# Kernel tuning notes

Measured on AMD Instinct MI355X. Metric: run time of the kernel, lower is better.

The kernel has to match this reference:

```python
import jax, jax.numpy as jnp
import numpy as np

F = 64  # dim_features
DIM_TASK = 32


def setup_inputs() -> dict:
    key = jax.random.key(0)
    ks = jax.random.split(key, 16)
    n_state, n_task, n_actor = 65536, 32768, 32768
    E_st, E_ta = 2_000_000, 1_000_000
    inp = {
        'x_state': jax.random.normal(ks[0], (n_state, F), jnp.float32),
        'x_task': jax.random.normal(ks[1], (n_task, F), jnp.float32),
        'x_actor': jax.random.normal(ks[2], (n_actor, F), jnp.float32),
        'edge_attr': jax.random.normal(ks[3], (E_st, 2), jnp.float32),
        # GINEConv edge linear: Linear(2 -> F)
        'We': jax.random.normal(ks[4], (2, F), jnp.float32) * 0.5,
        'be': jnp.zeros((F,), jnp.float32),
        # GinStandardMLP: Linear(F,F) -> ReLU -> Linear(F,F)
        'W1a': jax.random.normal(ks[5], (F, F), jnp.float32) / np.sqrt(F),
        'b1a': jnp.zeros((F,), jnp.float32),
        'W1b': jax.random.normal(ks[6], (F, F), jnp.float32) / np.sqrt(F),
        'b1b': jnp.zeros((F,), jnp.float32),
        # UnactivatedMLP: Linear(F,F) -> ReLU -> Linear(F,1)
        'W2a': jax.random.normal(ks[7], (F, F), jnp.float32) / np.sqrt(F),
        'b2a': jnp.zeros((F,), jnp.float32),
        'W2b': jax.random.normal(ks[8], (F, 1), jnp.float32) / np.sqrt(F),
        'b2b': jnp.zeros((1,), jnp.float32),
        'src_st': jax.random.randint(ks[9], (E_st,), 0, n_state, jnp.int32),
        'dst_st': jax.random.randint(ks[10], (E_st,), 0, n_task, jnp.int32),
        'src_ta': jax.random.randint(ks[11], (E_ta,), 0, n_task, jnp.int32),
        'dst_ta': jax.random.randint(ks[12], (E_ta,), 0, n_actor, jnp.int32),
    }
    return inp


def reference(x_state, x_task, x_actor, edge_attr, We, be, W1a, b1a, W1b, b1b,
              W2a, b2a, W2b, b2b, src_st, dst_st, src_ta, dst_ta):
    n_task = x_task.shape[0]
    n_actor = x_actor.shape[0]
    # --- GINEConv (eps=0): agg_i = sum_e relu(x_src[e] + lin(edge_attr[e])) ---
    msg = jax.nn.relu(x_state[src_st] + edge_attr @ We + be)  # [E_st, F]
    agg = jax.ops.segment_sum(msg, dst_st, num_segments=n_task)  # [n_task, F]
    h = x_task + agg  # (1+eps)*x_r + agg, eps=0
    # GinStandardMLP: Linear-ReLU-Linear
    x1 = jax.nn.relu(h @ W1a + b1a) @ W1b + b1b  # [n_task, F]
    # --- GINConv (eps=0): agg2_i = sum_e x1[src[e]] ---
    agg2 = jax.ops.segment_sum(x1[src_ta], dst_ta, num_segments=n_actor)  # [n_actor, F]
    h2 = x_actor + agg2
    # UnactivatedMLP: Linear-ReLU-Linear -> 1
    logits = jax.nn.relu(h2 @ W2a + b2a) @ W2b + b2b  # [n_actor, 1]
    return logits.reshape(-1, DIM_TASK)
```

## Files before the change

kernel.cpp:

```cpp
#include <hip/hip_runtime.h>

#define F 64
#define TILE 4096
#define NB 1024
#define ROWSB 32
#define CAP1 2560
#define CAP2 1408

typedef __attribute__((ext_vector_type(8))) short bf8;
typedef __attribute__((ext_vector_type(4))) float f4;
typedef __attribute__((ext_vector_type(2))) float fl2;

__device__ __forceinline__ unsigned short f2bf(float f) {
    unsigned u = __float_as_uint(f);
    unsigned r = u + 0x7fffu + ((u >> 16) & 1u);
    return (unsigned short)(r >> 16);
}
__device__ __forceinline__ float bf2f(unsigned short h) {
    return __uint_as_float((unsigned)h << 16);
}
__device__ __forceinline__ fl2 unpack2(unsigned d) {
    fl2 r;
    r.x = __uint_as_float(d << 16);
    r.y = __uint_as_float(d & 0xffff0000u);
    return r;
}

__global__ __launch_bounds__(1024) void prep_kernel(
    const float4* __restrict__ xs4, ushort4* __restrict__ xsb4, int n4,
    const int* __restrict__ src1, const int* __restrict__ dst1,
    const float* __restrict__ ea, int E1,
    int* __restrict__ cur1, uint2* __restrict__ keyA1,
    const int* __restrict__ src2, const int* __restrict__ dst2, int E2,
    int* __restrict__ cur2, unsigned* __restrict__ keyA2,
    int nCvt, int nBin1)
{
    __shared__ uint2 stage[TILE];
    __shared__ int hist[NB], scanb[NB], lstart[NB], lcur[NB], gbase[NB];
    int bid = blockIdx.x;
    int tid = threadIdx.x;

    if (bid < nCvt) {
        int i = bid * 1024 + tid;
        if (i < n4) {
            float4 v = xs4[i];
            ushort4 o;
            o.x = f2bf(v.x); o.y = f2bf(v.y); o.z = f2bf(v.z); o.w = f2bf(v.w);
            xsb4[i] = o;
        }
        return;
    }

    if (bid < nCvt + nBin1) {
        int base = (bid - nCvt) * TILE;
        int cnt = min(TILE, E1 - base);
        hist[tid] = 0;
        __syncthreads();
        int myb[4];
        #pragma unroll
        for (int j = 0; j < 4; ++j) {
            int idx = tid + 1024 * j;
            if (idx < cnt) {
                int b = dst1[base + idx] >> 5;
                myb[j] = b;
                atomicAdd(&hist[b], 1);
            } else myb[j] = -1;
        }
        __syncthreads();
        int c = hist[tid];
        gbase[tid] = CAP1 * tid + atomicAdd(&cur1[tid], c);
        scanb[tid] = c;
        __syncthreads();
        for (int off = 1; off < NB; off <<= 1) {
            int u = (tid >= off) ? scanb[tid - off] : 0;
            __syncthreads();
            scanb[tid] += u;
            __syncthreads();
        }
        int excl = scanb[tid] - c;
        lstart[tid] = excl;
        lcur[tid] = excl;
        __syncthreads();
        #pragma unroll
        for (int j = 0; j < 4; ++j) {
            int idx = tid + 1024 * j;
            if (idx < cnt) {
                int b = myb[j];
                int p = atomicAdd(&lcur[b], 1);
                float2 e2 = ((const float2* __restrict__)ea)[base + idx];
                unsigned sd = ((unsigned)src1[base + idx] << 16) | (unsigned)dst1[base + idx];
                unsigned pk = ((unsigned)f2bf(e2.y) << 16) | (unsigned)f2bf(e2.x);
                stage[p] = make_uint2(sd, pk);
            }
        }
        __syncthreads();
        #pragma unroll
        for (int j = 0; j < 4; ++j) {
            int p = tid + 1024 * j;
            if (p < cnt) {
                uint2 f = stage[p];
                int b = (int)(f.x & 0xffffu) >> 5;
                keyA1[gbase[b] + (p - lstart[b])] = f;
            }
        }
        return;
    }

    {
        unsigned* ustage = (unsigned*)stage;
        int base = (bid - nCvt - nBin1) * TILE;
        int cnt = min(TILE, E2 - base);
        hist[tid] = 0;
        __syncthreads();
        int myb[4];
        #pragma unroll
        for (int j = 0; j < 4; ++j) {
            int idx = tid + 1024 * j;
            if (idx < cnt) {
                int b = dst2[base + idx] >> 5;
                myb[j] = b;
                atomicAdd(&hist[b], 1);
            } else myb[j] = -1;
        }
        __syncthreads();
        int c = hist[tid];
        gbase[tid] = CAP2 * tid + atomicAdd(&cur2[tid], c);
        scanb[tid] = c;
        __syncthreads();
        for (int off = 1; off < NB; off <<= 1) {
            int u = (tid >= off) ? scanb[tid - off] : 0;
            __syncthreads();
            scanb[tid] += u;
            __syncthreads();
        }
        int excl = scanb[tid] - c;
        lstart[tid] = excl;
        lcur[tid] = excl;
        __syncthreads();
        #pragma unroll
        for (int j = 0; j < 4; ++j) {
            int idx = tid + 1024 * j;
            if (idx < cnt) {
                int b = myb[j];
                int p = atomicAdd(&lcur[b], 1);
                ustage[p] = ((unsigned)src2[base + idx] << 16) | (unsigned)dst2[base + idx];
            }
        }
        __syncthreads();
        #pragma unroll
        for (int j = 0; j < 4; ++j) {
            int p = tid + 1024 * j;
            if (p < cnt) {
                unsigned f = ustage[p];
                int b = (int)(f & 0xffffu) >> 5;
                keyA2[gbase[b] + (p - lstart[b])] = f;
            }
        }
    }
}

__global__ __launch_bounds__(512) void sg1_kernel(
    const uint2* __restrict__ keyA,
    const ushort* __restrict__ xsb,
    const float* __restrict__ x_task,
    const float* __restrict__ We, const float* __restrict__ be,
    const int* __restrict__ gcursor,
    float* __restrict__ hout, int n)
{
    __shared__ uint2 lpay[CAP1];
    __shared__ int hh[ROWSB], rst[ROWSB], cur[ROWSB];
    __shared__ float hbuf[8][F + 4];
    int tid = threadIdx.x;
    int b = blockIdx.x;
    int cnt = min(gcursor[b], CAP1);
    const uint2* ka = keyA + (size_t)b * CAP1;

    if (tid < ROWSB) hh[tid] = 0;
    __syncthreads();

    uint2 myk[5];
    #pragma unroll
    for (int j = 0; j < 5; ++j) {
        int idx = tid + 512 * j;
        if (idx < cnt) {
            myk[j] = ka[idx];
            atomicAdd(&hh[myk[j].x & 31u], 1);
        }
    }
    __syncthreads();
    if (tid < ROWSB) cur[tid] = hh[tid];
    __syncthreads();
    for (int off = 1; off < ROWSB; off <<= 1) {
        int u = (tid < ROWSB && tid >= off) ? cur[tid - off] : 0;
        __syncthreads();
        if (tid < ROWSB) cur[tid] += u;
        __syncthreads();
    }
    if (tid < ROWSB) {
        int excl = cur[tid] - hh[tid];
        rst[tid] = excl;
        cur[tid] = excl;
    }
    __syncthreads();
    #pragma unroll
    for (int j = 0; j < 5; ++j) {
        int idx = tid + 512 * j;
        if (idx < cnt) {
            int p = atomicAdd(&cur[myk[j].x & 31u], 1);
            lpay[p] = myk[j];
        }
    }
    __syncthreads();

    int wave = tid >> 6, lane = tid & 63;
    int q = lane & 7, g = lane >> 3;
    fl2 w0p[4], w1p[4], bbp[4];
    {
        float4 a0 = ((const float4* __restrict__)We)[q * 2];
        float4 a1 = ((const float4* __restrict__)We)[q * 2 + 1];
        float4 c0 = ((const float4* __restrict__)(We + F))[q * 2];
        float4 c1 = ((const float4* __restrict__)(We + F))[q * 2 + 1];
        float4 d0 = ((const float4* __restrict__)be)[q * 2];
        float4 d1 = ((const float4* __restrict__)be)[q * 2 + 1];
        w0p[0] = (fl2){a0.x, a0.y}; w0p[1] = (fl2){a0.z, a0.w};
        w0p[2] = (fl2){a1.x, a1.y}; w0p[3] = (fl2){a1.z, a1.w};
        w1p[0] = (fl2){c0.x, c0.y}; w1p[1] = (fl2){c0.z, c0.w};
        w1p[2] = (fl2){c1.x, c1.y}; w1p[3] = (fl2){c1.z, c1.w};
        bbp[0] = (fl2){d0.x, d0.y}; bbp[1] = (fl2){d0.z, d0.w};
        bbp[2] = (fl2){d1.x, d1.y}; bbp[3] = (fl2){d1.z, d1.w};
    }
    const fl2 zero2 = {0.f, 0.f};

    for (int r = wave; r < ROWSB; r += 8) {
        int row = b * ROWSB + r;
        if (row >= n) break;
        int start = rst[r];
        int c = hh[r];
        fl2 acc2[4];
        #pragma unroll
        for (int p = 0; p < 4; ++p) acc2[p] = zero2;

        #define SG1_BODY(ii)                                                     \
        {                                                                        \
            uint2 pe = lpay[start + (ii)];                                       \
            int s = (int)(pe.x >> 16);                                           \
            fl2 ex = {__uint_as_float(pe.y << 16), __uint_as_float(pe.y << 16)}; \
            fl2 ey = {__uint_as_float(pe.y & 0xffff0000u),                       \
                      __uint_as_float(pe.y & 0xffff0000u)};                      \
            uint4 xw = ((const uint4* __restrict__)(xsb + (size_t)s * F))[q];    \
            fl2 cc, t;                                                           \
            cc = __builtin_elementwise_fma(ey, w1p[0], bbp[0]);                  \
            cc = __builtin_elementwise_fma(ex, w0p[0], cc);                      \
            t = unpack2(xw.x) + cc;                                              \
            acc2[0] += __builtin_elementwise_max(t, zero2);                      \
            cc = __builtin_elementwise_fma(ey, w1p[1], bbp[1]);                  \
            cc = __builtin_elementwise_fma(ex, w0p[1], cc);                      \
            t = unpack2(xw.y) + cc;                                              \
            acc2[1] += __builtin_elementwise_max(t, zero2);                      \
            cc = __builtin_elementwise_fma(ey, w1p[2], bbp[2]);                  \
            cc = __builtin_elementwise_fma(ex, w0p[2], cc);                      \
            t = unpack2(xw.z) + cc;                                              \
            acc2[2] += __builtin_elementwise_max(t, zero2);                      \
            cc = __builtin_elementwise_fma(ey, w1p[3], bbp[3]);                  \
            cc = __builtin_elementwise_fma(ex, w0p[3], cc);                      \
            t = unpack2(xw.w) + cc;                                              \
            acc2[3] += __builtin_elementwise_max(t, zero2);                      \
        }

        int i = g;
        for (; i + 8 < c; i += 16) { SG1_BODY(i); SG1_BODY(i + 8); }
        for (; i < c; i += 8) SG1_BODY(i);
        #undef SG1_BODY

        float acc[8];
        #pragma unroll
        for (int p = 0; p < 4; ++p) { acc[2 * p] = acc2[p].x; acc[2 * p + 1] = acc2[p].y; }
        #pragma unroll
        for (int j = 0; j < 8; ++j) {
            acc[j] += __shfl_xor(acc[j], 8);
            acc[j] += __shfl_xor(acc[j], 16);
            acc[j] += __shfl_xor(acc[j], 32);
        }
        if (g == 0) {
            #pragma unroll
            for (int j = 0; j < 8; ++j)
                hbuf[wave][q * 8 + j] = acc[j];
        }
        float h = hbuf[wave][lane] + x_task[(size_t)row * F + lane];
        hout[(size_t)row * F + lane] = h;
    }
}

__global__ __launch_bounds__(256) void mlp1_kernel(
    const float* __restrict__ hin,
    const float* __restrict__ W1a, const float* __restrict__ b1a,
    const float* __restrict__ W1b, const float* __restrict__ b1b,
    ushort* __restrict__ x1b, int n)
{
    __shared__ float ldsH[4][16 * 68];
    int tid = threadIdx.x;
    int wave = tid >> 6, lane = tid & 63;
    int quad = lane >> 4, col = lane & 15;
    int rowbase = blockIdx.x * 64 + wave * 16;
    if (rowbase >= n) return;
    float* ltile = ldsH[wave];

    bf8 Wah[2][4], Wal[2][4], Wbh[2][4], Wbl[2][4];
    float ba1[4], bb1[4];
    #pragma unroll
    for (int kh = 0; kh < 2; ++kh)
        #pragma unroll
        for (int c = 0; c < 4; ++c) {
            bf8 th, tl, sh, sl;
            #pragma unroll
            for (int j = 0; j < 8; ++j) {
                int k = kh * 32 + quad * 8 + j;
                float wa = W1a[k * F + c * 16 + col];
                unsigned short h1 = f2bf(wa);
                th[j] = (short)h1; tl[j] = (short)f2bf(wa - bf2f(h1));
                float wb = W1b[k * F + c * 16 + col];
                unsigned short h2 = f2bf(wb);
                sh[j] = (short)h2; sl[j] = (short)f2bf(wb - bf2f(h2));
            }
            Wah[kh][c] = th; Wal[kh][c] = tl;
            Wbh[kh][c] = sh; Wbl[kh][c] = sl;
        }
    #pragma unroll
    for (int c = 0; c < 4; ++c) { ba1[c] = b1a[c * 16 + col]; bb1[c] = b1b[c * 16 + col]; }

    const float* hrow = hin + (size_t)(rowbase + col) * F + quad * 8;
    bf8 Ah[2], Al[2];
    #pragma unroll
    for (int kh = 0; kh < 2; ++kh) {
        bf8 th, tl;
        #pragma unroll
        for (int j = 0; j < 8; ++j) {
            float a = hrow[kh * 32 + j];
            unsigned short h1 = f2bf(a);
            th[j] = (short)h1; tl[j] = (short)f2bf(a - bf2f(h1));
        }
        Ah[kh] = th; Al[kh] = tl;
    }

    #pragma unroll
    for (int c = 0; c < 4; ++c) {
        f4 acc = {0.f, 0.f, 0.f, 0.f};
        #pragma unroll
        for (int kh = 0; kh < 2; ++kh) {
            acc = __builtin_amdgcn_mfma_f32_16x16x32_bf16(Ah[kh], Wah[kh][c], acc, 0, 0, 0);
            acc = __builtin_amdgcn_mfma_f32_16x16x32_bf16(Ah[kh], Wal[kh][c], acc, 0, 0, 0);
            acc = __builtin_amdgcn_mfma_f32_16x16x32_bf16(Al[kh], Wah[kh][c], acc, 0, 0, 0);
        }
        #pragma unroll
        for (int r = 0; r < 4; ++r)
            ltile[(quad * 4 + r) * 68 + c * 16 + col] = fmaxf(acc[r] + ba1[c], 0.f);
    }
    bf8 A2h[2], A2l[2];
    #pragma unroll
    for (int kh = 0; kh < 2; ++kh) {
        bf8 th, tl;
        #pragma unroll
        for (int j = 0; j < 8; ++j) {
            float a = ltile[col * 68 + kh * 32 + quad * 8 + j];
            unsigned short h1 = f2bf(a);
            th[j] = (short)h1; tl[j] = (short)f2bf(a - bf2f(h1));
        }
        A2h[kh] = th; A2l[kh] = tl;
    }
    #pragma unroll
    for (int c = 0; c < 4; ++c) {
        f4 acc = {0.f, 0.f, 0.f, 0.f};
        #pragma unroll
        for (int kh = 0; kh < 2; ++kh) {
            acc = __builtin_amdgcn_mfma_f32_16x16x32_bf16(A2h[kh], Wbh[kh][c], acc, 0, 0, 0);
            acc = __builtin_amdgcn_mfma_f32_16x16x32_bf16(A2h[kh], Wbl[kh][c], acc, 0, 0, 0);
            acc = __builtin_amdgcn_mfma_f32_16x16x32_bf16(A2l[kh], Wbh[kh][c], acc, 0, 0, 0);
        }
        #pragma unroll
        for (int r = 0; r < 4; ++r)
            ltile[(quad * 4 + r) * 68 + c * 16 + col] = acc[r] + bb1[c];
    }
    int rr = lane >> 2, cc = (lane & 3) * 16;
    unsigned o[8];
    #pragma unroll
    for (int j = 0; j < 8; ++j) {
        unsigned lo = f2bf(ltile[rr * 68 + cc + 2 * j]);
        unsigned hi = f2bf(ltile[rr * 68 + cc + 2 * j + 1]);
        o[j] = lo | (hi << 16);
    }
    uint4* dst = (uint4*)(x1b + (size_t)(rowbase + rr) * F + cc);
    dst[0] = make_uint4(o[0], o[1], o[2], o[3]);
    dst[1] = make_uint4(o[4], o[5], o[6], o[7]);
}

__global__ __launch_bounds__(512) void sg2_kernel(
    const unsigned* __restrict__ keyA,
    const ushort* __restrict__ x1b,
    const float* __restrict__ x_actor,
    const int* __restrict__ gcursor,
    float* __restrict__ h2out, int n)
{
    __shared__ unsigned lpay[CAP2];
    __shared__ int hh[ROWSB], rst[ROWSB], cur[ROWSB];
    __shared__ float hbuf[8][F + 4];
    int tid = threadIdx.x;
    int b = blockIdx.x;
    int cnt = min(gcursor[b], CAP2);
    const unsigned* ka = keyA + (size_t)b * CAP2;

    if (tid < ROWSB) hh[tid] = 0;
    __syncthreads();

    unsigned myk[3];
    #pragma unroll
    for (int j = 0; j < 3; ++j) {
        int idx = tid + 512 * j;
        if (idx < cnt) {
            myk[j] = ka[idx];
            atomicAdd(&hh[myk[j] & 31u], 1);
        }
    }
    __syncthreads();
    if (tid < ROWSB) cur[tid] = hh[tid];
    __syncthreads();
    for (int off = 1; off < ROWSB; off <<= 1) {
        int u = (tid < ROWSB && tid >= off) ? cur[tid - off] : 0;
        __syncthreads();
        if (tid < ROWSB) cur[tid] += u;
        __syncthreads();
    }
    if (tid < ROWSB) {
        int excl = cur[tid] - hh[tid];
        rst[tid] = excl;
        cur[tid] = excl;
    }
    __syncthreads();
    #pragma unroll
    for (int j = 0; j < 3; ++j) {
        int idx = tid + 512 * j;
        if (idx < cnt) {
            int p = atomicAdd(&cur[myk[j] & 31u], 1);
            lpay[p] = myk[j];
        }
    }
    __syncthreads();

    int wave = tid >> 6, lane = tid & 63;
    int q = lane & 7, g = lane >> 3;
    const fl2 zero2 = {0.f, 0.f};
    for (int r = wave; r < ROWSB; r += 8) {
        int row = b * ROWSB + r;
        if (row >= n) break;
        int start = rst[r];
        int c = hh[r];
        fl2 acc2[4];
        #pragma unroll
        for (int p = 0; p < 4; ++p) acc2[p] = zero2;

        #define SG2_BODY(ii)                                                  \
        {                                                                     \
            unsigned sd = lpay[start + (ii)];                                 \
            int s = (int)(sd >> 16);                                          \
            uint4 xw = ((const uint4* __restrict__)(x1b + (size_t)s * F))[q]; \
            acc2[0] += unpack2(xw.x);                                         \
            acc2[1] += unpack2(xw.y);                                         \
            acc2[2] += unpack2(xw.z);                                         \
            acc2[3] += unpack2(xw.w);                                         \
        }

        int i = g;
        for (; i + 8 < c; i += 16) { SG2_BODY(i); SG2_BODY(i + 8); }
        for (; i < c; i += 8) SG2_BODY(i);
        #undef SG2_BODY

        float acc[8];
        #pragma unroll
        for (int p = 0; p < 4; ++p) { acc[2 * p] = acc2[p].x; acc[2 * p + 1] = acc2[p].y; }
        #pragma unroll
        for (int j = 0; j < 8; ++j) {
            acc[j] += __shfl_xor(acc[j], 8);
            acc[j] += __shfl_xor(acc[j], 16);
            acc[j] += __shfl_xor(acc[j], 32);
        }
        if (g == 0) {
            #pragma unroll
            for (int j = 0; j < 8; ++j)
                hbuf[wave][q * 8 + j] = acc[j];
        }
        float h = hbuf[wave][lane] + x_actor[(size_t)row * F + lane];
        h2out[(size_t)row * F + lane] = h;
    }
}

__global__ __launch_bounds__(256) void mlp2_kernel(
    const float* __restrict__ h2in,
    const float* __restrict__ W2a, const float* __restrict__ b2a,
    const float* __restrict__ W2b, const float* __restrict__ b2b,
    float* __restrict__ out, int n)
{
    int tid = threadIdx.x;
    int wave = tid >> 6, lane = tid & 63;
    int quad = lane >> 4, col = lane & 15;
    int rowbase = blockIdx.x * 64 + wave * 16;
    if (rowbase >= n) return;

    bf8 Wah[2][4], Wal[2][4];
    float ba1[4], wo[4];
    #pragma unroll
    for (int kh = 0; kh < 2; ++kh)
        #pragma unroll
        for (int c = 0; c < 4; ++c) {
            bf8 th, tl;
            #pragma unroll
            for (int j = 0; j < 8; ++j) {
                int k = kh * 32 + quad * 8 + j;
                float w = W2a[k * F + c * 16 + col];
                unsigned short h1 = f2bf(w);
                th[j] = (short)h1; tl[j] = (short)f2bf(w - bf2f(h1));
            }
            Wah[kh][c] = th; Wal[kh][c] = tl;
        }
    #pragma unroll
    for (int c = 0; c < 4; ++c) { ba1[c] = b2a[c * 16 + col]; wo[c] = W2b[c * 16 + col]; }
    float bias2 = b2b[0];

    const float* hrow = h2in + (size_t)(rowbase + col) * F + quad * 8;
    bf8 Ah[2], Al[2];
    #pragma unroll
    for (int kh = 0; kh < 2; ++kh) {
        bf8 th, tl;
        #pragma unroll
        for (int j = 0; j < 8; ++j) {
            float a = hrow[kh * 32 + j];
            unsigned short h1 = f2bf(a);
            th[j] = (short)h1; tl[j] = (short)f2bf(a - bf2f(h1));
        }
        Ah[kh] = th; Al[kh] = tl;
    }

    float partial[4] = {0.f, 0.f, 0.f, 0.f};
    #pragma unroll
    for (int c = 0; c < 4; ++c) {
        f4 acc = {0.f, 0.f, 0.f, 0.f};
        #pragma unroll
        for (int kh = 0; kh < 2; ++kh) {
            acc = __builtin_amdgcn_mfma_f32_16x16x32_bf16(Ah[kh], Wah[kh][c], acc, 0, 0, 0);
            acc = __builtin_amdgcn_mfma_f32_16x16x32_bf16(Ah[kh], Wal[kh][c], acc, 0, 0, 0);
            acc = __builtin_amdgcn_mfma_f32_16x16x32_bf16(Al[kh], Wah[kh][c], acc, 0, 0, 0);
        }
        #pragma unroll
        for (int r = 0; r < 4; ++r)
            partial[r] += fmaxf(acc[r] + ba1[c], 0.f) * wo[c];
    }
    #pragma unroll
    for (int off = 1; off < 16; off <<= 1)
        #pragma unroll
        for (int r = 0; r < 4; ++r)
            partial[r] += __shfl_xor(partial[r], off);
    if (col == 0) {
        #pragma unroll
        for (int r = 0; r < 4; ++r)
            out[rowbase + quad * 4 + r] = partial[r] + bias2;
    }
}

extern "C" void kernel_launch(void* const* d_in, const int* in_sizes, int n_in,
                              void* d_out, int out_size, void* d_ws, size_t ws_size,
                              hipStream_t stream)
{
    const float* x_state   = (const float*)d_in[0];
    const float* x_task    = (const float*)d_in[1];
    const float* x_actor   = (const float*)d_in[2];
    const float* edge_attr = (const float*)d_in[3];
    const float* We        = (const float*)d_in[4];
    const float* be        = (const float*)d_in[5];
    const float* W1a       = (const float*)d_in[6];
    const float* b1a       = (const float*)d_in[7];
    const float* W1b       = (const float*)d_in[8];
    const float* b1b       = (const float*)d_in[9];
    const float* W2a       = (const float*)d_in[10];
    const float* b2a       = (const float*)d_in[11];
    const float* W2b       = (const float*)d_in[12];
    const float* b2b       = (const float*)d_in[13];
    const int*   src_st    = (const int*)d_in[14];
    const int*   dst_st    = (const int*)d_in[15];
    const int*   src_ta    = (const int*)d_in[16];
    const int*   dst_ta    = (const int*)d_in[17];

    int n_state = in_sizes[0] / F;
    int n_task  = in_sizes[1] / F;
    int n_actor = in_sizes[2] / F;
    int E_st    = in_sizes[14];
    int E_ta    = in_sizes[16];

    ushort*   x1b   = (ushort*)d_ws;
    float*    hbig  = (float*)(x1b + (size_t)n_task * F);
    ushort*   xsb   = (ushort*)(hbig + (size_t)n_task * F);
    uint2*    keyA1 = (uint2*)(xsb + (size_t)n_state * F);
    unsigned* keyA2 = (unsigned*)(keyA1 + (size_t)NB * CAP1);
    int*      cur1  = (int*)(keyA2 + (size_t)NB * CAP2);
    int*      cur2  = cur1 + NB;

    int n4    = n_state * F / 4;
    int nCvt  = (n4 + 1023) / 1024;
    int nBin1 = (E_st + TILE - 1) / TILE;
    int nBin2 = (E_ta + TILE - 1) / TILE;

    hipMemsetAsync(cur1, 0, 2 * NB * sizeof(int), stream);
    prep_kernel<<<nCvt + nBin1 + nBin2, 1024, 0, stream>>>(
        (const float4*)x_state, (ushort4*)xsb, n4,
        src_st, dst_st, edge_attr, E_st, cur1, keyA1,
        src_ta, dst_ta, E_ta, cur2, keyA2,
        nCvt, nBin1);
    sg1_kernel<<<NB, 512, 0, stream>>>(
        keyA1, xsb, x_task, We, be, cur1, hbig, n_task);
    mlp1_kernel<<<(n_task + 63) / 64, 256, 0, stream>>>(
        hbig, W1a, b1a, W1b, b1b, x1b, n_task);
    sg2_kernel<<<NB, 512, 0, stream>>>(
        keyA2, x1b, x_actor, cur2, hbig, n_actor);
    mlp2_kernel<<<(n_actor + 63) / 64, 256, 0, stream>>>(
        hbig, W2a, b2a, W2b, b2b, (float*)d_out, n_actor);
}
```

Baseline: 227.2 us.

## Fuse GIN MLPs into segment-gather kernels via shared-memory row tiles

Merges mlp1 into sg1 and mlp2 into sg2. Each block now keeps its 32 aggregated rows in an LDS tile, stages the weight matrices through LDS (reusing the payload buffer), and runs the MFMA MLP in place. This removes two kernel launches and the fp32 round-trip of h/h2 through global memory. In exchange only 2 of 8 waves do the MLP work, and every block reloads and re-splits the weights, so the block tail gets longer.

```diff
diff --git a/kernel.cpp b/kernel.cpp
--- a/kernel.cpp
+++ b/kernel.cpp
@@ -164,12 +164,17 @@
     const ushort* __restrict__ xsb,
     const float* __restrict__ x_task,
     const float* __restrict__ We, const float* __restrict__ be,
+    const float* __restrict__ W1a, const float* __restrict__ b1a,
+    const float* __restrict__ W1b, const float* __restrict__ b1b,
     const int* __restrict__ gcursor,
-    float* __restrict__ hout, int n)
+    ushort* __restrict__ x1b, int n)
 {
-    __shared__ uint2 lpay[CAP1];
+    __shared__ __align__(16) char smemraw[CAP1 * 8];
+    __shared__ float htile[ROWSB * 68];
     __shared__ int hh[ROWSB], rst[ROWSB], cur[ROWSB];
-    __shared__ float hbuf[8][F + 4];
+    uint2* lpay = (uint2*)smemraw;
+    float* ldsW = (float*)smemraw;
+
     int tid = threadIdx.x;
     int b = blockIdx.x;
     int cnt = min(gcursor[b], CAP1);
@@ -284,125 +289,131 @@
         if (g == 0) {
             #pragma unroll
             for (int j = 0; j < 8; ++j)
-                hbuf[wave][q * 8 + j] = acc[j];
-        }
-        float h = hbuf[wave][lane] + x_task[(size_t)row * F + lane];
-        hout[(size_t)row * F + lane] = h;
-    }
-}
-
-__global__ __launch_bounds__(256) void mlp1_kernel(
-    const float* __restrict__ hin,
-    const float* __restrict__ W1a, const float* __restrict__ b1a,
-    const float* __restrict__ W1b, const float* __restrict__ b1b,
-    ushort* __restrict__ x1b, int n)
-{
-    __shared__ float ldsH[4][16 * 68];
-    int tid = threadIdx.x;
-    int wave = tid >> 6, lane = tid & 63;
+                htile[r * 68 + q * 8 + j] = acc[j];
+        }
+        float h = htile[r * 68 + lane] + x_task[(size_t)row * F + lane];
+        htile[r * 68 + lane] = h;
+    }
+    __syncthreads();
+
+    for (int i = tid; i < F * F; i += 512) ldsW[i] = W1a[i];
+    __syncthreads();
+
     int quad = lane >> 4, col = lane & 15;
-    int rowbase = blockIdx.x * 64 + wave * 16;
-    if (rowbase >= n) return;
-    float* ltile = ldsH[wave];
-
-    bf8 Wah[2][4], Wal[2][4], Wbh[2][4], Wbl[2][4];
-    float ba1[4], bb1[4];
-    #pragma unroll
-    for (int kh = 0; kh < 2; ++kh)
+    int rb = wave * 16;
+    bf8 A2h[2], A2l[2];
+
+    if (wave < 2) {
+        #pragma unroll
+        for (int kh = 0; kh < 2; ++kh) {
+            bf8 th, tl;
+            #pragma unroll
+            for (int j = 0; j < 8; ++j) {
+                float a = htile[(rb + col) * 68 + kh * 32 + quad * 8 + j];
+                unsigned short h1 = f2bf(a);
+                th[j] = (short)h1; tl[j] = (short)f2bf(a - bf2f(h1));
+            }
+            A2h[kh] = th; A2l[kh] = tl;
+        }
         #pragma unroll
         for (int c = 0; c < 4; ++c) {
-            bf8 th, tl, sh, sl;
+            bf8 Bh[2], Bl[2];
+            #pragma unroll
+            for (int kh = 0; kh < 2; ++kh) {
+                bf8 sh, sl;
+                #pragma unroll
+                for (int j = 0; j < 8; ++j) {
+                    float w = ldsW[(kh * 32 + quad * 8 + j) * F + c * 16 + col];
+                    unsigned short h1 = f2bf(w);
+                    sh[j] = (short)h1; sl[j] = (short)f2bf(w - bf2f(h1));
+                }
+                Bh[kh] = sh; Bl[kh] = sl;
+            }
+            f4 acc = {0.f, 0.f, 0.f, 0.f};
+            #pragma unroll
+            for (int kh = 0; kh < 2; ++kh) {
+                acc = __builtin_amdgcn_mfma_f32_16x16x32_bf16(A2h[kh], Bh[kh], acc, 0, 0, 0);
+                acc = __builtin_amdgcn_mfma_f32_16x16x32_bf16(A2h[kh], Bl[kh], acc, 0, 0, 0);
+                acc = __builtin_amdgcn_mfma_f32_16x16x32_bf16(A2l[kh], Bh[kh], acc, 0, 0, 0);
+            }
+            float ba = b1a[c * 16 + col];
+            #pragma unroll
+            for (int r = 0; r < 4; ++r)
+                htile[(rb + quad * 4 + r) * 68 + c * 16 + col] = fmaxf(acc[r] + ba, 0.f);
+        }
+    }
+    __syncthreads();
+    for (int i = tid; i < F * F; i += 512) ldsW[i] = W1b[i];
+    __syncthreads();
+
+    if (wave < 2) {
+        #pragma unroll
+        for (int kh = 0; kh < 2; ++kh) {
+            bf8 th, tl;
             #pragma unroll
             for (int j = 0; j < 8; ++j) {
-                int k = kh * 32 + quad * 8 + j;
-                float wa = W1a[k * F + c * 16 + col];
-                unsigned short h1 = f2bf(wa);
-                th[j] = (short)h1; tl[j] = (short)f2bf(wa - bf2f(h1));
-                float wb = W1b[k * F + c * 16 + col];
-                unsigned short h2 = f2bf(wb);
-                sh[j] = (short)h2; sl[j] = (short)f2bf(wb - bf2f(h2));
-            }
-            Wah[kh][c] = th; Wal[kh][c] = tl;
-            Wbh[kh][c] = sh; Wbl[kh][c] = sl;
-        }
-    #pragma unroll
-    for (int c = 0; c < 4; ++c) { ba1[c] = b1a[c * 16 + col]; bb1[c] = b1b[c * 16 + col]; }
-
-    const float* hrow = hin + (size_t)(rowbase + col) * F + quad * 8;
-    bf8 Ah[2], Al[2];
-    #pragma unroll
-    for (int kh = 0; kh < 2; ++kh) {
-        bf8 th, tl;
-        #pragma unroll
-        for (int j = 0; j < 8; ++j) {
-            float a = hrow[kh * 32 + j];
-            unsigned short h1 = f2bf(a);
-            th[j] = (short)h1; tl[j] = (short)f2bf(a - bf2f(h1));
-        }
-        Ah[kh] = th; Al[kh] = tl;
-    }
-
-    #pragma unroll
-    for (int c = 0; c < 4; ++c) {
-        f4 acc = {0.f, 0.f, 0.f, 0.f};
-        #pragma unroll
-        for (int kh = 0; kh < 2; ++kh) {
-            acc = __builtin_amdgcn_mfma_f32_16x16x32_bf16(Ah[kh], Wah[kh][c], acc, 0, 0, 0);
-            acc = __builtin_amdgcn_mfma_f32_16x16x32_bf16(Ah[kh], Wal[kh][c], acc, 0, 0, 0);
-            acc = __builtin_amdgcn_mfma_f32_16x16x32_bf16(Al[kh], Wah[kh][c], acc, 0, 0, 0);
-        }
-        #pragma unroll
-        for (int r = 0; r < 4; ++r)
-            ltile[(quad * 4 + r) * 68 + c * 16 + col] = fmaxf(acc[r] + ba1[c], 0.f);
-    }
-    bf8 A2h[2], A2l[2];
-    #pragma unroll
-    for (int kh = 0; kh < 2; ++kh) {
-        bf8 th, tl;
-        #pragma unroll
-        for (int j = 0; j < 8; ++j) {
-            float a = ltile[col * 68 + kh * 32 + quad * 8 + j];
-            unsigned short h1 = f2bf(a);
-            th[j] = (short)h1; tl[j] = (short)f2bf(a - bf2f(h1));
-        }
-        A2h[kh] = th; A2l[kh] = tl;
-    }
-    #pragma unroll
-    for (int c = 0; c < 4; ++c) {
-        f4 acc = {0.f, 0.f, 0.f, 0.f};
-        #pragma unroll
-        for (int kh = 0; kh < 2; ++kh) {
-            acc = __builtin_amdgcn_mfma_f32_16x16x32_bf16(A2h[kh], Wbh[kh][c], acc, 0, 0, 0);
-            acc = __builtin_amdgcn_mfma_f32_16x16x32_bf16(A2h[kh], Wbl[kh][c], acc, 0, 0, 0);
-            acc = __builtin_amdgcn_mfma_f32_16x16x32_bf16(A2l[kh], Wbh[kh][c], acc, 0, 0, 0);
-        }
-        #pragma unroll
-        for (int r = 0; r < 4; ++r)
-            ltile[(quad * 4 + r) * 68 + c * 16 + col] = acc[r] + bb1[c];
-    }
-    int rr = lane >> 2, cc = (lane & 3) * 16;
-    unsigned o[8];
-    #pragma unroll
-    for (int j = 0; j < 8; ++j) {
-        unsigned lo = f2bf(ltile[rr * 68 + cc + 2 * j]);
-        unsigned hi = f2bf(ltile[rr * 68 + cc + 2 * j + 1]);
-        o[j] = lo | (hi << 16);
-    }
-    uint4* dst = (uint4*)(x1b + (size_t)(rowbase + rr) * F + cc);
-    dst[0] = make_uint4(o[0], o[1], o[2], o[3]);
-    dst[1] = make_uint4(o[4], o[5], o[6], o[7]);
+                float a = htile[(rb + col) * 68 + kh * 32 + quad * 8 + j];
+                unsigned short h1 = f2bf(a);
+                th[j] = (short)h1; tl[j] = (short)f2bf(a - bf2f(h1));
+            }
+            A2h[kh] = th; A2l[kh] = tl;
+        }
+        #pragma unroll
+        for (int c = 0; c < 4; ++c) {
+            bf8 Bh[2], Bl[2];
+            #pragma unroll
+            for (int kh = 0; kh < 2; ++kh) {
+                bf8 sh, sl;
+                #pragma unroll
+                for (int j = 0; j < 8; ++j) {
+                    float w = ldsW[(kh * 32 + quad * 8 + j) * F + c * 16 + col];
+                    unsigned short h1 = f2bf(w);
+                    sh[j] = (short)h1; sl[j] = (short)f2bf(w - bf2f(h1));
+                }
+                Bh[kh] = sh; Bl[kh] = sl;
+            }
+            f4 acc = {0.f, 0.f, 0.f, 0.f};
+            #pragma unroll
+            for (int kh = 0; kh < 2; ++kh) {
+                acc = __builtin_amdgcn_mfma_f32_16x16x32_bf16(A2h[kh], Bh[kh], acc, 0, 0, 0);
+                acc = __builtin_amdgcn_mfma_f32_16x16x32_bf16(A2h[kh], Bl[kh], acc, 0, 0, 0);
+                acc = __builtin_amdgcn_mfma_f32_16x16x32_bf16(A2l[kh], Bh[kh], acc, 0, 0, 0);
+            }
+            float bbv = b1b[c * 16 + col];
+            #pragma unroll
+            for (int r = 0; r < 4; ++r)
+                htile[(rb + quad * 4 + r) * 68 + c * 16 + col] = acc[r] + bbv;
+        }
+        int rr = lane >> 2, cc2 = (lane & 3) * 16;
+        int row = b * ROWSB + rb + rr;
+        if (row < n) {
+            unsigned o[8];
+            #pragma unroll
+            for (int j = 0; j < 8; ++j) {
+                unsigned lo = f2bf(htile[(rb + rr) * 68 + cc2 + 2 * j]);
+                unsigned hi = f2bf(htile[(rb + rr) * 68 + cc2 + 2 * j + 1]);
+                o[j] = lo | (hi << 16);
+            }
+            uint4* dst = (uint4*)(x1b + (size_t)row * F + cc2);
+            dst[0] = make_uint4(o[0], o[1], o[2], o[3]);
+            dst[1] = make_uint4(o[4], o[5], o[6], o[7]);
+        }
+    }
 }
 
 __global__ __launch_bounds__(512) void sg2_kernel(
     const unsigned* __restrict__ keyA,
     const ushort* __restrict__ x1b,
     const float* __restrict__ x_actor,
+    const float* __restrict__ W2a, const float* __restrict__ b2a,
+    const float* __restrict__ W2b, const float* __restrict__ b2b,
     const int* __restrict__ gcursor,
-    float* __restrict__ h2out, int n)
+    float* __restrict__ out, int n)
 {
     __shared__ unsigned lpay[CAP2];
+    __shared__ float ldsW[F * F];
+    __shared__ float htile[ROWSB * 68];
     __shared__ int hh[ROWSB], rst[ROWSB], cur[ROWSB];
-    __shared__ float hbuf[8][F + 4];
     int tid = threadIdx.x;
     int b = blockIdx.x;
     int cnt = min(gcursor[b], CAP2);
@@ -485,82 +496,72 @@
         if (g == 0) {
             #pragma unroll
             for (int j = 0; j < 8; ++j)
-                hbuf[wave][q * 8 + j] = acc[j];
-        }
-        float h = hbuf[wave][lane] + x_actor[(size_t)row * F + lane];
-        h2out[(size_t)row * F + lane] = h;
-    }
-}
-
-__global__ __launch_bounds__(256) void mlp2_kernel(
-    const float* __restrict__ h2in,
-    const float* __restrict__ W2a, const float* __restrict__ b2a,
-    const float* __restrict__ W2b, const float* __restrict__ b2b,
-    float* __restrict__ out, int n)
-{
-    int tid = threadIdx.x;
-    int wave = tid >> 6, lane = tid & 63;
-    int quad = lane >> 4, col = lane & 15;
-    int rowbase = blockIdx.x * 64 + wave * 16;
-    if (rowbase >= n) return;
-
-    bf8 Wah[2][4], Wal[2][4];
-    float ba1[4], wo[4];
-    #pragma unroll
-    for (int kh = 0; kh < 2; ++kh)
+                htile[r * 68 + q * 8 + j] = acc[j];
+        }
+        float h = htile[r * 68 + lane] + x_actor[(size_t)row * F + lane];
+        htile[r * 68 + lane] = h;
+    }
+    __syncthreads();
+
+    for (int i = tid; i < F * F; i += 512) ldsW[i] = W2a[i];
+    __syncthreads();
+
+    if (wave < 2) {
+        int quad = lane >> 4, col = lane & 15;
+        int rb = wave * 16;
+        bf8 Ah[2], Al[2];
+        #pragma unroll
+        for (int kh = 0; kh < 2; ++kh) {
+            bf8 th, tl;
+            #pragma unroll
+            for (int j = 0; j < 8; ++j) {
+                float a = htile[(rb + col) * 68 + kh * 32 + quad * 8 + j];
+                unsigned short h1 = f2bf(a);
+                th[j] = (short)h1; tl[j] = (short)f2bf(a - bf2f(h1));
+            }
+            Ah[kh] = th; Al[kh] = tl;
+        }
+        float partial[4] = {0.f, 0.f, 0.f, 0.f};
         #pragma unroll
         for (int c = 0; c < 4; ++c) {
-            bf8 th, tl;
-            #pragma unroll
-            for (int j = 0; j < 8; ++j) {
-                int k = kh * 32 + quad * 8 + j;
-                float w = W2a[k * F + c * 16 + col];
-                unsigned short h1 = f2bf(w);
-                th[j] = (short)h1; tl[j] = (short)f2bf(w - bf2f(h1));
-            }
-            Wah[kh][c] = th; Wal[kh][c] = tl;
-        }
-    #pragma unroll
-    for (int c = 0; c < 4; ++c) { ba1[c] = b2a[c * 16 + col]; wo[c] = W2b[c * 16 + col]; }
-    float bias2 = b2b[0];
-
-    const float* hrow = h2in + (size_t)(rowbase + col) * F + quad * 8;
-    bf8 Ah[2], Al[2];
-    #pragma unroll
-    for (int kh = 0; kh < 2; ++kh) {
-        bf8 th, tl;
-        #pragma unroll
-        for (int j = 0; j < 8; ++j) {
-            float a = hrow[kh * 32 + j];
-            unsigned short h1 = f2bf(a);
-            th[j] = (short)h1; tl[j] = (short)f2bf(a - bf2f(h1));
-        }
-        Ah[kh] = th; Al[kh] = tl;
-    }
-
-    float partial[4] = {0.f, 0.f, 0.f, 0.f};
-    #pragma unroll
-    for (int c = 0; c < 4; ++c) {
-        f4 acc = {0.f, 0.f, 0.f, 0.f};
-        #pragma unroll
-        for (int kh = 0; kh < 2; ++kh) {
-            acc = __builtin_amdgcn_mfma_f32_16x16x32_bf16(Ah[kh], Wah[kh][c], acc, 0, 0, 0);
-            acc = __builtin_amdgcn_mfma_f32_16x16x32_bf16(Ah[kh], Wal[kh][c], acc, 0, 0, 0);
-            acc = __builtin_amdgcn_mfma_f32_16x16x32_bf16(Al[kh], Wah[kh][c], acc, 0, 0, 0);
-        }
-        #pragma unroll
-        for (int r = 0; r < 4; ++r)
-            partial[r] += fmaxf(acc[r] + ba1[c], 0.f) * wo[c];
-    }
-    #pragma unroll
-    for (int off = 1; off < 16; off <<= 1)
-        #pragma unroll
-        for (int r = 0; r < 4; ++r)
-            partial[r] += __shfl_xor(partial[r], off);
-    if (col == 0) {
-        #pragma unroll
-        for (int r = 0; r < 4; ++r)
-            out[rowbase + quad * 4 + r] = partial[r] + bias2;
+            bf8 Bh[2], Bl[2];
+            #pragma unroll
+            for (int kh = 0; kh < 2; ++kh) {
+                bf8 sh, sl;
+                #pragma unroll
+                for (int j = 0; j < 8; ++j) {
+                    float w = ldsW[(kh * 32 + quad * 8 + j) * F + c * 16 + col];
+                    unsigned short h1 = f2bf(w);
+                    sh[j] = (short)h1; sl[j] = (short)f2bf(w - bf2f(h1));
+                }
+                Bh[kh] = sh; Bl[kh] = sl;
+            }
+            f4 acc = {0.f, 0.f, 0.f, 0.f};
+            #pragma unroll
+            for (int kh = 0; kh < 2; ++kh) {
+                acc = __builtin_amdgcn_mfma_f32_16x16x32_bf16(Ah[kh], Bh[kh], acc, 0, 0, 0);
+                acc = __builtin_amdgcn_mfma_f32_16x16x32_bf16(Ah[kh], Bl[kh], acc, 0, 0, 0);
+                acc = __builtin_amdgcn_mfma_f32_16x16x32_bf16(Al[kh], Bh[kh], acc, 0, 0, 0);
+            }
+            float ba = b2a[c * 16 + col];
+            float wo = W2b[c * 16 + col];
+            #pragma unroll
+            for (int r = 0; r < 4; ++r)
+                partial[r] += fmaxf(acc[r] + ba, 0.f) * wo;
+        }
+        #pragma unroll
+        for (int off = 1; off < 16; off <<= 1)
+            #pragma unroll
+            for (int r = 0; r < 4; ++r)
+                partial[r] += __shfl_xor(partial[r], off);
+        if (col == 0) {
+            float bias2 = b2b[0];
+            #pragma unroll
+            for (int r = 0; r < 4; ++r) {
+                int row = b * ROWSB + rb + quad * 4 + r;
+                if (row < n) out[row] = partial[r] + bias2;
+            }
+        }
     }
 }
 
@@ -594,8 +595,7 @@
     int E_ta    = in_sizes[16];
 
     ushort*   x1b   = (ushort*)d_ws;
-    float*    hbig  = (float*)(x1b + (size_t)n_task * F);
-    ushort*   xsb   = (ushort*)(hbig + (size_t)n_task * F);
+    ushort*   xsb   = x1b + (size_t)n_task * F;
     uint2*    keyA1 = (uint2*)(xsb + (size_t)n_state * F);
     unsigned* keyA2 = (unsigned*)(keyA1 + (size_t)NB * CAP1);
     int*      cur1  = (int*)(keyA2 + (size_t)NB * CAP2);
@@ -613,11 +613,9 @@
         src_ta, dst_ta, E_ta, cur2, keyA2,
         nCvt, nBin1);
     sg1_kernel<<<NB, 512, 0, stream>>>(
-        keyA1, xsb, x_task, We, be, cur1, hbig, n_task);
-    mlp1_kernel<<<(n_task + 63) / 64, 256, 0, stream>>>(
-        hbig, W1a, b1a, W1b, b1b, x1b, n_task);
+        keyA1, xsb, x_task, We, be, W1a, b1a, W1b, b1b,
+        cur1, x1b, n_task);
     sg2_kernel<<<NB, 512, 0, stream>>>(
-        keyA2, x1b, x_actor, cur2, hbig, n_actor);
-    mlp2_kernel<<<(n_actor + 63) / 64, 256, 0, stream>>>(
-        hbig, W2a, b2a, W2b, b2b, (float*)d_out, n_actor);
+        keyA2, x1b, x_actor, W2a, b2a, W2b, b2b,
+        cur2, (float*)d_out, n_actor);
 }
```

Measured after the change: 240.4 us. +5.8%, slower.
